# Kernel tuning notes

Hardware: AMD Instinct MI355X
Metric: run time of the kernel (lower is better)

## Reference

```python
import jax, jax.numpy as jnp
import numpy as np

RADIUS = 2.0
DECAY = 1.0


def setup_inputs() -> dict:
    key = jax.random.key(0)
    k1, k2 = jax.random.split(key)
    x = jax.random.normal(k1, (2048, 16), dtype=jnp.float32)
    data = jax.random.normal(k2, (65536, 16), dtype=jnp.float32)
    return {"x": x, "data": data}


def reference(x, data):
    # Brute-force L2 nearest-neighbor (faiss IndexFlatL2 / IVF nlist=1 == exact search)
    # dist2[q, n] = ||x_q - data_n||^2, via the expansion trick.
    x2 = jnp.sum(x * x, axis=1, keepdims=True)            # [Nq, 1]
    d2 = jnp.sum(data * data, axis=1)                      # [Nd]
    dist2 = x2 + d2[None, :] - 2.0 * (x @ data.T)          # [Nq, Nd] -- dominant traffic
    nn2 = jnp.maximum(jnp.min(dist2, axis=1), 0.0)         # clamp tiny negatives from cancellation
    dist = jnp.sqrt(jnp.maximum(nn2, 1e-12))               # sqrt of squared L2, squeeze(k=1)

    # bump_above(dist, RADIUS, DECAY):
    #   inside mask: exp(decay / (d^2 - r^2)) / exp(-decay / r^2)
    #   outside: 0
    r2 = RADIUS * RADIUS
    mask = jnp.abs(dist) < RADIUS
    denom = jnp.where(mask, dist * dist - r2, -1.0)        # safe denom outside mask
    bump = jnp.where(mask, jnp.exp(DECAY / denom + DECAY / r2), 0.0)
    return bump
```

## Files before the change

kernel.cpp:

```cpp
#include <hip/hip_runtime.h>
#include <float.h>
#include <math.h>

constexpr int NQ = 2048;
constexpr int ND = 65536;
constexpr int D  = 16;

constexpr int SCH = 64;
constexpr int CP  = ND / SCH;
constexpr int TPW = CP / 32;

typedef short bf16x8 __attribute__((ext_vector_type(8)));
typedef float f32x16 __attribute__((ext_vector_type(16)));

__device__ __forceinline__ unsigned short f2bf(float f) {
    unsigned u = __float_as_uint(f);
    u += 0x7FFFu + ((u >> 16) & 1u);
    return (unsigned short)(u >> 16);
}
__device__ __forceinline__ float bf2f(unsigned short h) {
    return __uint_as_float(((unsigned)h) << 16);
}

__global__ __launch_bounds__(256) void pack_inputs(const float* __restrict__ x,
                                                   const float* __restrict__ data,
                                                   unsigned short* __restrict__ Ppk,
                                                   unsigned short* __restrict__ Apk,
                                                   float* __restrict__ nhf) {
    const int idx = blockIdx.x * 256 + threadIdx.x;
    const float* src;
    unsigned short* dst;
    if (idx < ND) {
        src = data + (size_t)idx * D;
        dst = Ppk + (size_t)idx * 32;
    } else {
        const int q = idx - ND;
        if (q >= NQ) return;
        src = x + (size_t)q * D;
        dst = Apk + (size_t)q * 32;
    }
    const float4* r4 = (const float4*)src;
    float4 a = r4[0], b = r4[1], c = r4[2], e = r4[3];
    float v[16] = {a.x, a.y, a.z, a.w, b.x, b.y, b.z, b.w,
                   c.x, c.y, c.z, c.w, e.x, e.y, e.z, e.w};
    unsigned short row[32];
    float n = 0.f;
#pragma unroll
    for (int k = 0; k < 16; ++k) {
        n = fmaf(v[k], v[k], n);
        unsigned short h = f2bf(v[k]);
        row[k]      = h;
        row[16 + k] = f2bf(v[k] - bf2f(h));
    }
    uint4* w4 = (uint4*)dst;
    const uint4* r = (const uint4*)row;
    w4[0] = r[0]; w4[1] = r[1]; w4[2] = r[2]; w4[3] = r[3];
    if (idx < ND) nhf[idx] = -0.5f * n;
}

__global__ __launch_bounds__(256) void knn_mfma(const unsigned short* __restrict__ Apk,
                                                const unsigned short* __restrict__ Ppk,
                                                const float* __restrict__ nhf,
                                                float* __restrict__ part) {
    const int tid  = threadIdx.x;
    const int w    = tid >> 6;
    const int l    = tid & 63;
    const int half = l >> 5;
    const int n31  = l & 31;
    const int qbase = blockIdx.x * 128 + w * 32;
    const int pbase = blockIdx.y * CP;

    const int m = qbase + n31;
    bf16x8 axh = *(const bf16x8*)(Apk + (size_t)m * 32 + half * 8);
    bf16x8 axl = *(const bf16x8*)(Apk + (size_t)m * 32 + 16 + half * 8);

    const unsigned short* bp = Ppk + (size_t)(pbase + n31) * 32 + half * 8;
    const float*          np = nhf + pbase + n31;

    f32x16 rbest;
#pragma unroll
    for (int r = 0; r < 16; ++r) rbest[r] = -FLT_MAX;

    bf16x8 bh = *(const bf16x8*)bp;
    bf16x8 bl = *(const bf16x8*)(bp + 16);
    float  nv = *np;
    bp += 32 * 32;  np += 32;

    for (int t = 0; t < TPW; ++t) {
        bf16x8 nbh, nbl; float nnv;
        if (t + 1 < TPW) {
            nbh = *(const bf16x8*)bp;
            nbl = *(const bf16x8*)(bp + 16);
            nnv = *np;
            bp += 32 * 32;  np += 32;
        }
        f32x16 c;
#pragma unroll
        for (int r = 0; r < 16; ++r) c[r] = nv;
        c = __builtin_amdgcn_mfma_f32_32x32x16_bf16(axh, bh, c, 0, 0, 0);
        c = __builtin_amdgcn_mfma_f32_32x32x16_bf16(axl, bh, c, 0, 0, 0);
        c = __builtin_amdgcn_mfma_f32_32x32x16_bf16(axh, bl, c, 0, 0, 0);
#pragma unroll
        for (int r = 0; r < 16; ++r) rbest[r] = fmaxf(rbest[r], c[r]);
        bh = nbh; bl = nbl; nv = nnv;
    }

#pragma unroll
    for (int r = 0; r < 16; ++r) {
        float v = rbest[r];
        v = fmaxf(v, __shfl_xor(v, 1, 32));
        v = fmaxf(v, __shfl_xor(v, 2, 32));
        v = fmaxf(v, __shfl_xor(v, 4, 32));
        v = fmaxf(v, __shfl_xor(v, 8, 32));
        v = fmaxf(v, __shfl_xor(v, 16, 32));
        rbest[r] = v;
    }
    if (n31 == 0) {
        float* pp = part + (size_t)blockIdx.y * NQ + qbase + 4 * half;
#pragma unroll
        for (int r = 0; r < 16; ++r) pp[(r & 3) + 8 * (r >> 2)] = rbest[r];
    }
}

__global__ __launch_bounds__(256) void knn_final_mfma(const float* __restrict__ x,
                                                      const float* __restrict__ part,
                                                      float* __restrict__ out) {
    const int q = blockIdx.x * 256 + threadIdx.x;
    const float4* xr = (const float4*)(x + (size_t)q * D);
    float4 a = xr[0], b = xr[1], c = xr[2], e = xr[3];
    float x2 = a.x * a.x;
    x2 = fmaf(a.y, a.y, x2); x2 = fmaf(a.z, a.z, x2); x2 = fmaf(a.w, a.w, x2);
    x2 = fmaf(b.x, b.x, x2); x2 = fmaf(b.y, b.y, x2); x2 = fmaf(b.z, b.z, x2); x2 = fmaf(b.w, b.w, x2);
    x2 = fmaf(c.x, c.x, x2); x2 = fmaf(c.y, c.y, x2); x2 = fmaf(c.z, c.z, x2); x2 = fmaf(c.w, c.w, x2);
    x2 = fmaf(e.x, e.x, x2); x2 = fmaf(e.y, e.y, x2); x2 = fmaf(e.z, e.z, x2); x2 = fmaf(e.w, e.w, x2);

    float mbest = -FLT_MAX;
#pragma unroll
    for (int cI = 0; cI < SCH; ++cI) mbest = fmaxf(mbest, part[(size_t)cI * NQ + q]);

    float nn2  = fmaxf(fmaf(-2.f, mbest, x2), 0.f);
    float dist = sqrtf(fmaxf(nn2, 1e-12f));
    float bump = 0.f;
    if (dist < 2.0f) {
        float denom = dist * dist - 4.0f;
        bump = expf(1.0f / denom + 0.25f);
    }
    out[q] = bump;
}

__global__ __launch_bounds__(256) void neg_half_norms(const float* __restrict__ data,
                                                      float* __restrict__ nhn) {
    const int p = blockIdx.x * 256 + threadIdx.x;
    const float4* r = (const float4*)(data + (size_t)p * D);
    float4 a = r[0], b = r[1], c = r[2], e = r[3];
    float n = a.x * a.x;
    n = fmaf(a.y, a.y, n); n = fmaf(a.z, a.z, n); n = fmaf(a.w, a.w, n);
    n = fmaf(b.x, b.x, n); n = fmaf(b.y, b.y, n); n = fmaf(b.z, b.z, n); n = fmaf(b.w, b.w, n);
    n = fmaf(c.x, c.x, n); n = fmaf(c.y, c.y, n); n = fmaf(c.z, c.z, n); n = fmaf(c.w, c.w, n);
    n = fmaf(e.x, e.x, n); n = fmaf(e.y, e.y, n); n = fmaf(e.z, e.z, n); n = fmaf(e.w, e.w, n);
    nhn[p] = -0.5f * n;
}

__global__ __launch_bounds__(256) void knn_partial_fb(const float* __restrict__ x,
                                                      const float* __restrict__ data,
                                                      const float* __restrict__ nhn,
                                                      float* __restrict__ part, int cp) {
    const int q     = blockIdx.x * 256 + threadIdx.x;
    const int pbase = blockIdx.y * cp;
    const float4* xr = (const float4*)(x + (size_t)q * D);
    const float4 xa = xr[0], xb = xr[1], xc = xr[2], xd = xr[3];
    const float* dp = data + (size_t)pbase * D;
    const float* np = nhn + pbase;
    float best = -FLT_MAX;
    for (int i = 0; i < cp; i += 4) {
#pragma unroll
        for (int j = 0; j < 4; ++j) {
            const float* r  = dp + (size_t)(i + j) * D;
            const float  hn = np[i + j];
            float ca = xa.x * r[0];
            ca = fmaf(xa.y, r[1], ca);  ca = fmaf(xa.z, r[2], ca);  ca = fmaf(xa.w, r[3], ca);
            ca = fmaf(xb.x, r[4], ca);  ca = fmaf(xb.y, r[5], ca);  ca = fmaf(xb.z, r[6], ca);
            ca = fmaf(xb.w, r[7], ca);
            float cb = fmaf(xc.x, r[8], hn);
            cb = fmaf(xc.y, r[9],  cb); cb = fmaf(xc.z, r[10], cb); cb = fmaf(xc.w, r[11], cb);
            cb = fmaf(xd.x, r[12], cb); cb = fmaf(xd.y, r[13], cb); cb = fmaf(xd.z, r[14], cb);
            cb = fmaf(xd.w, r[15], cb);
            best = fmaxf(best, ca + cb);
        }
    }
    part[(size_t)blockIdx.y * NQ + q] = best;
}

__global__ __launch_bounds__(256) void knn_final_fb(const float* __restrict__ x,
                                                    const float* __restrict__ part,
                                                    float* __restrict__ out, int S) {
    const int q = blockIdx.x * 256 + threadIdx.x;
    const float4* xr = (const float4*)(x + (size_t)q * D);
    float4 a = xr[0], b = xr[1], c = xr[2], e = xr[3];
    float x2 = a.x * a.x;
    x2 = fmaf(a.y, a.y, x2); x2 = fmaf(a.z, a.z, x2); x2 = fmaf(a.w, a.w, x2);
    x2 = fmaf(b.x, b.x, x2); x2 = fmaf(b.y, b.y, x2); x2 = fmaf(b.z, b.z, x2); x2 = fmaf(b.w, b.w, x2);
    x2 = fmaf(c.x, c.x, x2); x2 = fmaf(c.y, c.y, x2); x2 = fmaf(c.z, c.z, x2); x2 = fmaf(c.w, c.w, x2);
    x2 = fmaf(e.x, e.x, x2); x2 = fmaf(e.y, e.y, x2); x2 = fmaf(e.z, e.z, x2); x2 = fmaf(e.w, e.w, x2);
    float mb = -FLT_MAX;
    for (int cI = 0; cI < S; ++cI) mb = fmaxf(mb, part[(size_t)cI * NQ + q]);
    float nn2  = fmaxf(fmaf(-2.f, mb, x2), 0.f);
    float dist = sqrtf(fmaxf(nn2, 1e-12f));
    float bump = 0.f;
    if (dist < 2.0f) {
        float denom = dist * dist - 4.0f;
        bump = expf(1.0f / denom + 0.25f);
    }
    out[q] = bump;
}

extern "C" void kernel_launch(void* const* d_in, const int* in_sizes, int n_in,
                              void* d_out, int out_size, void* d_ws, size_t ws_size,
                              hipStream_t stream) {
    const float* x    = (const float*)d_in[0];
    const float* data = (const float*)d_in[1];
    float* out = (float*)d_out;

    const size_t off_Apk  = (size_t)ND * 32 * 2;
    const size_t off_nhf  = off_Apk + (size_t)NQ * 32 * 2;
    const size_t off_part = off_nhf + (size_t)ND * 4;
    const size_t needed   = off_part + (size_t)SCH * NQ * 4;

    if (ws_size >= needed) {
        unsigned short* Ppk = (unsigned short*)d_ws;
        unsigned short* Apk = (unsigned short*)((char*)d_ws + off_Apk);
        float* nhf  = (float*)((char*)d_ws + off_nhf);
        float* part = (float*)((char*)d_ws + off_part);

        pack_inputs<<<(ND + NQ) / 256, 256, 0, stream>>>(x, data, Ppk, Apk, nhf);
        knn_mfma<<<dim3(NQ / 128, SCH), 256, 0, stream>>>(Apk, Ppk, nhf, part);
        knn_final_mfma<<<NQ / 256, 256, 0, stream>>>(x, part, out);
    } else {
        int S = 32;
        while (S > 1 && (size_t)(ND + S * NQ) * sizeof(float) > ws_size) S >>= 1;
        const int cp = ND / S;
        float* nhn  = (float*)d_ws;
        float* part = (float*)d_ws + ND;
        neg_half_norms<<<ND / 256, 256, 0, stream>>>(data, nhn);
        knn_partial_fb<<<dim3(NQ / 256, S), 256, 0, stream>>>(x, data, nhn, part, cp);
        knn_final_fb<<<NQ / 256, 256, 0, stream>>>(x, part, out, S);
    }
}
```

Baseline: 90.35 us.

## Interleave two MFMA tiles per step with double-buffered loads; pack queries in-kernel

The main loop now handles pairs of 32-point tiles. The two independent MFMA chains are interleaved to hide MFMA dependency latency, and the next pair is loaded in a ping-pong scheme while the current pair computes. Query bf16 hi/lo splitting moves from the pack kernel into the knn kernel, so the packed query buffer disappears. Launch bounds now request 4 blocks per CU. The cost is more registers held for two accumulators and eight operand vectors, which may strain occupancy.

New measurement: 85.05 us. 5.9% less time.

```diff
diff --git a/kernel.cpp b/kernel.cpp
--- a/kernel.cpp
+++ b/kernel.cpp
@@ -6,9 +6,10 @@
 constexpr int ND = 65536;
 constexpr int D  = 16;
 
-constexpr int SCH = 64;
-constexpr int CP  = ND / SCH;
-constexpr int TPW = CP / 32;
+constexpr int SCH   = 64;
+constexpr int CP    = ND / SCH;
+constexpr int TPW   = CP / 32;
+constexpr int NPAIR = TPW / 2;
 
 typedef short bf16x8 __attribute__((ext_vector_type(8)));
 typedef float f32x16 __attribute__((ext_vector_type(16)));
@@ -22,24 +23,11 @@
     return __uint_as_float(((unsigned)h) << 16);
 }
 
-__global__ __launch_bounds__(256) void pack_inputs(const float* __restrict__ x,
-                                                   const float* __restrict__ data,
-                                                   unsigned short* __restrict__ Ppk,
-                                                   unsigned short* __restrict__ Apk,
-                                                   float* __restrict__ nhf) {
-    const int idx = blockIdx.x * 256 + threadIdx.x;
-    const float* src;
-    unsigned short* dst;
-    if (idx < ND) {
-        src = data + (size_t)idx * D;
-        dst = Ppk + (size_t)idx * 32;
-    } else {
-        const int q = idx - ND;
-        if (q >= NQ) return;
-        src = x + (size_t)q * D;
-        dst = Apk + (size_t)q * 32;
-    }
-    const float4* r4 = (const float4*)src;
+__global__ __launch_bounds__(256) void pack_data(const float* __restrict__ data,
+                                                 unsigned short* __restrict__ Ppk,
+                                                 float* __restrict__ nhf) {
+    const int p = blockIdx.x * 256 + threadIdx.x;
+    const float4* r4 = (const float4*)(data + (size_t)p * D);
     float4 a = r4[0], b = r4[1], c = r4[2], e = r4[3];
     float v[16] = {a.x, a.y, a.z, a.w, b.x, b.y, b.z, b.w,
                    c.x, c.y, c.z, c.w, e.x, e.y, e.z, e.w};
@@ -52,16 +40,16 @@
         row[k]      = h;
         row[16 + k] = f2bf(v[k] - bf2f(h));
     }
-    uint4* w4 = (uint4*)dst;
-    const uint4* r = (const uint4*)row;
-    w4[0] = r[0]; w4[1] = r[1]; w4[2] = r[2]; w4[3] = r[3];
-    if (idx < ND) nhf[idx] = -0.5f * n;
-}
-
-__global__ __launch_bounds__(256) void knn_mfma(const unsigned short* __restrict__ Apk,
-                                                const unsigned short* __restrict__ Ppk,
-                                                const float* __restrict__ nhf,
-                                                float* __restrict__ part) {
+    uint4* w4 = (uint4*)(Ppk + (size_t)p * 32);
+    const uint4* rr = (const uint4*)row;
+    w4[0] = rr[0]; w4[1] = rr[1]; w4[2] = rr[2]; w4[3] = rr[3];
+    nhf[p] = -0.5f * n;
+}
+
+__global__ __launch_bounds__(256, 4) void knn_mfma(const float* __restrict__ x,
+                                                   const unsigned short* __restrict__ Ppk,
+                                                   const float* __restrict__ nhf,
+                                                   float* __restrict__ part) {
     const int tid  = threadIdx.x;
     const int w    = tid >> 6;
     const int l    = tid & 63;
@@ -70,40 +58,65 @@
     const int qbase = blockIdx.x * 128 + w * 32;
     const int pbase = blockIdx.y * CP;
 
-    const int m = qbase + n31;
-    bf16x8 axh = *(const bf16x8*)(Apk + (size_t)m * 32 + half * 8);
-    bf16x8 axl = *(const bf16x8*)(Apk + (size_t)m * 32 + 16 + half * 8);
+    const float* xr = x + (size_t)(qbase + n31) * D + half * 8;
+    float4 x0 = *(const float4*)xr;
+    float4 x1 = *(const float4*)(xr + 4);
+    const float xv[8] = {x0.x, x0.y, x0.z, x0.w, x1.x, x1.y, x1.z, x1.w};
+    bf16x8 axh, axl;
+#pragma unroll
+    for (int k = 0; k < 8; ++k) {
+        unsigned short h = f2bf(xv[k]);
+        axh[k] = (short)h;
+        axl[k] = (short)f2bf(xv[k] - bf2f(h));
+    }
 
     const unsigned short* bp = Ppk + (size_t)(pbase + n31) * 32 + half * 8;
     const float*          np = nhf + pbase + n31;
 
+#define LDH(t) (*(const bf16x8*)(bp + (size_t)(t) * 1024))
+#define LDL(t) (*(const bf16x8*)(bp + (size_t)(t) * 1024 + 16))
+#define LDN(t) (np[(size_t)(t) * 32])
+
     f32x16 rbest;
 #pragma unroll
     for (int r = 0; r < 16; ++r) rbest[r] = -FLT_MAX;
 
-    bf16x8 bh = *(const bf16x8*)bp;
-    bf16x8 bl = *(const bf16x8*)(bp + 16);
-    float  nv = *np;
-    bp += 32 * 32;  np += 32;
-
-    for (int t = 0; t < TPW; ++t) {
-        bf16x8 nbh, nbl; float nnv;
-        if (t + 1 < TPW) {
-            nbh = *(const bf16x8*)bp;
-            nbl = *(const bf16x8*)(bp + 16);
-            nnv = *np;
-            bp += 32 * 32;  np += 32;
+    auto compute_pair = [&](bf16x8 h0, bf16x8 l0, float n0,
+                            bf16x8 h1, bf16x8 l1, float n1) {
+        f32x16 c0, c1;
+#pragma unroll
+        for (int r = 0; r < 16; ++r) { c0[r] = n0; c1[r] = n1; }
+        c0 = __builtin_amdgcn_mfma_f32_32x32x16_bf16(axh, h0, c0, 0, 0, 0);
+        c1 = __builtin_amdgcn_mfma_f32_32x32x16_bf16(axh, h1, c1, 0, 0, 0);
+        c0 = __builtin_amdgcn_mfma_f32_32x32x16_bf16(axl, h0, c0, 0, 0, 0);
+        c1 = __builtin_amdgcn_mfma_f32_32x32x16_bf16(axl, h1, c1, 0, 0, 0);
+        c0 = __builtin_amdgcn_mfma_f32_32x32x16_bf16(axh, l0, c0, 0, 0, 0);
+        c1 = __builtin_amdgcn_mfma_f32_32x32x16_bf16(axh, l1, c1, 0, 0, 0);
+#pragma unroll
+        for (int r = 0; r < 16; ++r)
+            rbest[r] = fmaxf(rbest[r], fmaxf(c0[r], c1[r]));
+    };
+
+    bf16x8 Ah0 = LDH(0), Al0 = LDL(0), Ah1 = LDH(1), Al1 = LDL(1);
+    float  An0 = LDN(0), An1 = LDN(1);
+    bf16x8 Bh0, Bl0, Bh1, Bl1;
+    float  Bn0, Bn1;
+
+    for (int p = 0; p < NPAIR; p += 2) {
+        const int tB = (p + 1) * 2;
+        Bh0 = LDH(tB);     Bl0 = LDL(tB);     Bn0 = LDN(tB);
+        Bh1 = LDH(tB + 1); Bl1 = LDL(tB + 1); Bn1 = LDN(tB + 1);
+        compute_pair(Ah0, Al0, An0, Ah1, Al1, An1);
+        if (p + 2 < NPAIR) {
+            const int tA = (p + 2) * 2;
+            Ah0 = LDH(tA);     Al0 = LDL(tA);     An0 = LDN(tA);
+            Ah1 = LDH(tA + 1); Al1 = LDL(tA + 1); An1 = LDN(tA + 1);
         }
-        f32x16 c;
-#pragma unroll
-        for (int r = 0; r < 16; ++r) c[r] = nv;
-        c = __builtin_amdgcn_mfma_f32_32x32x16_bf16(axh, bh, c, 0, 0, 0);
-        c = __builtin_amdgcn_mfma_f32_32x32x16_bf16(axl, bh, c, 0, 0, 0);
-        c = __builtin_amdgcn_mfma_f32_32x32x16_bf16(axh, bl, c, 0, 0, 0);
-#pragma unroll
-        for (int r = 0; r < 16; ++r) rbest[r] = fmaxf(rbest[r], c[r]);
-        bh = nbh; bl = nbl; nv = nnv;
-    }
+        compute_pair(Bh0, Bl0, Bn0, Bh1, Bl1, Bn1);
+    }
+#undef LDH
+#undef LDL
+#undef LDN
 
 #pragma unroll
     for (int r = 0; r < 16; ++r) {
@@ -122,9 +135,9 @@
     }
 }
 
-__global__ __launch_bounds__(256) void knn_final_mfma(const float* __restrict__ x,
-                                                      const float* __restrict__ part,
-                                                      float* __restrict__ out) {
+__global__ __launch_bounds__(256) void knn_final(const float* __restrict__ x,
+                                                 const float* __restrict__ part,
+                                                 float* __restrict__ out) {
     const int q = blockIdx.x * 256 + threadIdx.x;
     const float4* xr = (const float4*)(x + (size_t)q * D);
     float4 a = xr[0], b = xr[1], c = xr[2], e = xr[3];
@@ -221,20 +234,18 @@
     const float* data = (const float*)d_in[1];
     float* out = (float*)d_out;
 
-    const size_t off_Apk  = (size_t)ND * 32 * 2;
-    const size_t off_nhf  = off_Apk + (size_t)NQ * 32 * 2;
+    const size_t off_nhf  = (size_t)ND * 32 * 2;
     const size_t off_part = off_nhf + (size_t)ND * 4;
     const size_t needed   = off_part + (size_t)SCH * NQ * 4;
 
     if (ws_size >= needed) {
         unsigned short* Ppk = (unsigned short*)d_ws;
-        unsigned short* Apk = (unsigned short*)((char*)d_ws + off_Apk);
         float* nhf  = (float*)((char*)d_ws + off_nhf);
         float* part = (float*)((char*)d_ws + off_part);
 
-        pack_inputs<<<(ND + NQ) / 256, 256, 0, stream>>>(x, data, Ppk, Apk, nhf);
-        knn_mfma<<<dim3(NQ / 128, SCH), 256, 0, stream>>>(Apk, Ppk, nhf, part);
-        knn_final_mfma<<<NQ / 256, 256, 0, stream>>>(x, part, out);
+        pack_data<<<ND / 256, 256, 0, stream>>>(data, Ppk, nhf);
+        knn_mfma<<<dim3(NQ / 128, SCH), 256, 0, stream>>>(x, Ppk, nhf, part);
+        knn_final<<<NQ / 256, 256, 0, stream>>>(x, part, out);
     } else {
         int S = 32;
         while (S > 1 && (size_t)(ND + S * NQ) * sizeof(float) > ws_size) S >>= 1;
```
